# Kernel optimization log

Measured on AMD Instinct MI355X. Metric: run time of the kernel, lower is better.

## Reference

```python
import jax, jax.numpy as jnp
import numpy as np

N = 100000   # nodes
E = 1600000  # edges (before self-loops)
F_IN = 128
H = 64
G = 512      # graphs in batch


def _add_self_loops(edge_index, n):
    loop = jnp.arange(n, dtype=edge_index.dtype)
    src = jnp.concatenate([edge_index[0], loop])
    dst = jnp.concatenate([edge_index[1], loop])
    return src, dst


def _gcn_norm(src, dst, n):
    # PyG GCNConv: deg over targets with self-loops, norm = d^-1/2[src]*d^-1/2[dst]
    deg = jax.ops.segment_sum(jnp.ones_like(dst, dtype=jnp.float32), dst, num_segments=n)
    dinv = jnp.where(deg > 0, jax.lax.rsqrt(deg), 0.0)
    return dinv[src] * dinv[dst]


def _gcn_conv(x, src, dst, norm, W, b):
    xw = x @ W                                # [N, H]
    msg = xw[src] * norm[:, None]             # [E+N, H] gather + scale
    out = jax.ops.segment_sum(msg, dst, num_segments=x.shape[0])
    return out + b


def setup_inputs() -> dict:
    key = jax.random.key(0)
    ks = jax.random.split(key, 9)
    x = jax.random.normal(ks[0], (N, F_IN), dtype=jnp.float32)
    edge_index = jax.random.randint(ks[1], (2, E), 0, N, dtype=jnp.int32)
    batch = jnp.sort(jax.random.randint(ks[2], (N,), 0, G, dtype=jnp.int32))
    s1 = 1.0 / np.sqrt(F_IN)
    s2 = 1.0 / np.sqrt(H)
    W1 = jax.random.uniform(ks[3], (F_IN, H), jnp.float32, -s1, s1)
    b1 = jnp.zeros((H,), jnp.float32)
    W2 = jax.random.uniform(ks[4], (H, H), jnp.float32, -s2, s2)
    b2 = jnp.zeros((H,), jnp.float32)
    Wl = jax.random.uniform(ks[5], (H, 1), jnp.float32, -s2, s2)
    bl = jnp.zeros((1,), jnp.float32)
    return {"x": x, "edge_index": edge_index, "batch": batch,
            "W1": W1, "b1": b1, "W2": W2, "b2": b2, "Wl": Wl, "bl": bl}


def reference(x, edge_index, batch, W1, b1, W2, b2, Wl, bl):
    n = x.shape[0]
    src, dst = _add_self_loops(edge_index, n)
    norm = _gcn_norm(src, dst, n)
    h = jax.nn.relu(_gcn_conv(x, src, dst, norm, W1, b1))
    h = jax.nn.relu(_gcn_conv(h, src, dst, norm, W2, b2))
    # global mean pool over graphs
    sums = jax.ops.segment_sum(h, batch, num_segments=G)          # [G, H]
    cnt = jax.ops.segment_sum(jnp.ones((n,), jnp.float32), batch, num_segments=G)
    pooled = sums / jnp.maximum(cnt, 1.0)[:, None]
    return jax.nn.sigmoid(pooled @ Wl + bl)                        # [G, 1]
```

## Files before the change

kernel.cpp:

```cpp
#include <hip/hip_runtime.h>
#include <hip/hip_bf16.h>
#include <cmath>

#define F_IN 128
#define HDIM 64
#define NPB 128
#define NB1 512
#define CAP 2560
#define GGRID 2048

typedef __attribute__((ext_vector_type(8))) short bf16x8;
typedef __attribute__((ext_vector_type(4))) float f32x4;
typedef __attribute__((ext_vector_type(2))) float f32x2;

__device__ __forceinline__ unsigned short f2bf(float f) {
    __hip_bfloat16 h = __float2bfloat16(f);
    union { __hip_bfloat16 h; unsigned short u; } c; c.h = h; return c.u;
}
__device__ __forceinline__ unsigned char f2fp8(float f) {
    int p = __builtin_amdgcn_cvt_pk_fp8_f32(f, f, 0, false);
    return (unsigned char)(p & 0xff);
}
__device__ __forceinline__ void fp8x8_acc(uint2 v, float* a) {
    f32x2 f;
    f = __builtin_amdgcn_cvt_pk_f32_fp8(v.x, false); a[0] += f.x; a[1] += f.y;
    f = __builtin_amdgcn_cvt_pk_f32_fp8(v.x, true);  a[2] += f.x; a[3] += f.y;
    f = __builtin_amdgcn_cvt_pk_f32_fp8(v.y, false); a[4] += f.x; a[5] += f.y;
    f = __builtin_amdgcn_cvt_pk_f32_fp8(v.y, true);  a[6] += f.x; a[7] += f.y;
}

__device__ __forceinline__ void gather_rows(const int* __restrict__ col,
                                            const uint2* __restrict__ xws,
                                            int L, int s, int end, float* a) {
    int e = s;
    for (; e + 8 <= end; e += 8) {
        uint2 v0 = xws[(size_t)col[e + 0] * 8 + L];
        uint2 v1 = xws[(size_t)col[e + 1] * 8 + L];
        uint2 v2 = xws[(size_t)col[e + 2] * 8 + L];
        uint2 v3 = xws[(size_t)col[e + 3] * 8 + L];
        uint2 v4 = xws[(size_t)col[e + 4] * 8 + L];
        uint2 v5 = xws[(size_t)col[e + 5] * 8 + L];
        uint2 v6 = xws[(size_t)col[e + 6] * 8 + L];
        uint2 v7 = xws[(size_t)col[e + 7] * 8 + L];
        fp8x8_acc(v0, a); fp8x8_acc(v1, a); fp8x8_acc(v2, a); fp8x8_acc(v3, a);
        fp8x8_acc(v4, a); fp8x8_acc(v5, a); fp8x8_acc(v6, a); fp8x8_acc(v7, a);
    }
    for (; e < end; ++e)
        fp8x8_acc(xws[(size_t)col[e] * 8 + L], a);
}

__device__ __forceinline__ int remap_group(int v, int nbuk) {
    int phase = v / nbuk;
    int b = v - phase * nbuk;
    return b * 4 + (3 - phase);
}


__launch_bounds__(256)
__global__ void k_init(const float* __restrict__ W1, const float* __restrict__ W2,
                       unsigned short* __restrict__ w1t, unsigned short* __restrict__ w2t,
                       const int* __restrict__ batch, int* __restrict__ gstart,
                       int n, int G, int* __restrict__ gcnt, int nbuk,
                       float* __restrict__ pooled) {
    int t = blockIdx.x * 256 + threadIdx.x;
    if (t < F_IN * 64) {
        int c = t & 63, k = t >> 6;
        w1t[c * F_IN + k] = f2bf(W1[t]);
        return;
    }
    t -= F_IN * 64;
    if (t < HDIM * 64) {
        int c = t & 63, k = t >> 6;
        w2t[c * HDIM + k] = f2bf(W2[t]);
        return;
    }
    t -= HDIM * 64;
    if (t <= G) {
        int g = t;
        int lo = 0, hi = n;
        while (lo < hi) {
            int mid = (lo + hi) >> 1;
            if (batch[mid] < g) lo = mid + 1; else hi = mid;
        }
        gstart[g] = lo;
        return;
    }
    t -= G + 1;
    if (t < nbuk) { gcnt[t] = 0; return; }
    t -= nbuk;
    if (t < G * HDIM) pooled[t] = 0.0f;
}


__launch_bounds__(256)
__global__ void p_place(const int* __restrict__ src, const int* __restrict__ dst,
                        int* __restrict__ gcnt, int* __restrict__ pairs,
                        int E, int nbuk, int chunk) {
    __shared__ int hist[1024];
    __shared__ int cur[1024];
    int tid = threadIdx.x;
    for (int i = tid; i < nbuk; i += 256) hist[i] = 0;
    __syncthreads();
    int lo = blockIdx.x * chunk, hi = min(E, lo + chunk);
    for (int e = lo + tid; e < hi; e += 256)
        atomicAdd(&hist[dst[e] >> 7], 1);
    __syncthreads();
    for (int i = tid; i < nbuk; i += 256) {
        int c = hist[i];
        cur[i] = i * CAP + (c ? atomicAdd(&gcnt[i], c) : 0);
    }
    __syncthreads();
    for (int e = lo + tid; e < hi; e += 256) {
        int d = dst[e];
        int pos = atomicAdd(&cur[d >> 7], 1);
        pairs[pos] = (src[e] << 7) | (d & 127);
    }
}


__launch_bounds__(256)
__global__ void p2_csr(const int* __restrict__ pairs, const int* __restrict__ bucket_cnt,
                       float* __restrict__ dinv, int* __restrict__ col,
                       int4* __restrict__ slot_hdr, int n) {
    __shared__ int plds[CAP];
    __shared__ int dl[128];
    __shared__ int sc[128];
    __shared__ int cur[128];
    __shared__ int h64[64];
    __shared__ int s64[64];
    int b = blockIdx.x, tid = threadIdx.x;
    int nlo = b << 7;
    int eb = b * CAP;
    int cnt = bucket_cnt[b];
    if (tid < 128) dl[tid] = 0;
    if (tid < 64) h64[tid] = 0;
    __syncthreads();
    for (int i = tid; i < cnt; i += 256) {
        int v = pairs[eb + i];
        plds[i] = v;
        atomicAdd(&dl[v & 127], 1);
    }
    __syncthreads();
    int d0 = 0, excl = 0;
    if (tid < 128) { d0 = dl[tid]; sc[tid] = d0; }
    __syncthreads();
    for (int off = 1; off < 128; off <<= 1) {
        int a = (tid >= off && tid < 128) ? sc[tid - off] : 0;
        __syncthreads();
        if (tid < 128) sc[tid] += a;
        __syncthreads();
    }
    if (tid < 128) {
        excl = sc[tid] - d0;
        int node = nlo + tid;
        float dv = rsqrtf((float)(d0 + 1));
        if (node < n) dinv[node] = dv;
        cur[tid] = eb + excl;
        atomicAdd(&h64[min(d0, 63)], 1);
    }
    __syncthreads();
    if (tid == 0) { int run = 0; for (int i = 0; i < 64; ++i) { s64[i] = run; run += h64[i]; } }
    __syncthreads();
    if (tid < 64) h64[tid] = 0;
    __syncthreads();
    if (tid < 128) {
        int node = nlo + tid;
        int bin = min(d0, 63);
        int pos = s64[bin] + atomicAdd(&h64[bin], 1);
        int4 hdr;
        hdr.x = (node < n) ? node : 0x7fffffff;
        hdr.y = eb + excl;
        hdr.z = d0;
        hdr.w = __float_as_int(rsqrtf((float)(d0 + 1)));
        slot_hdr[nlo + pos] = hdr;
    }
    __syncthreads();
    for (int i = tid; i < cnt; i += 256) {
        unsigned int v = (unsigned int)plds[i];
        int pos = atomicAdd(&cur[v & 127], 1);
        col[pos] = (int)(v >> 7);
    }
}


template <int K>
__launch_bounds__(256)
__global__ void matmul_mfma(const float* __restrict__ X, const unsigned short* __restrict__ Wt,
                            const float* __restrict__ dinv, unsigned char* __restrict__ out,
                            int n) {
    constexpr int KS  = K / 32;
    constexpr int LDX = K + 8;
    __shared__ unsigned short Xs[64 * LDX];
    __shared__ unsigned short Ws[64 * LDX];
    int tid = threadIdx.x;
    int rowbase = blockIdx.x * 64;
    for (int i = tid; i < 64 * (K / 8); i += 256) {
        int r = i / (K / 8), ch = i % (K / 8);
        *(bf16x8*)(Ws + r * LDX + ch * 8) = ((const bf16x8*)Wt)[i];
    }
    {
        const float4* X4 = (const float4*)X;
        for (int i = tid; i < 64 * (K / 4); i += 256) {
            int r = i / (K / 4), k4 = i % (K / 4);
            ushort4 u = { 0, 0, 0, 0 };
            int gr = rowbase + r;
            if (gr < n) {
                float4 v = X4[(size_t)gr * (K / 4) + k4];
                u.x = f2bf(v.x); u.y = f2bf(v.y); u.z = f2bf(v.z); u.w = f2bf(v.w);
            }
            *(ushort4*)(Xs + r * LDX + k4 * 4) = u;
        }
    }
    __syncthreads();
    int wave = tid >> 6, lane = tid & 63;
    int q = lane >> 4, nn = lane & 15;
    f32x4 acc[4] = {{0,0,0,0},{0,0,0,0},{0,0,0,0},{0,0,0,0}};
    int mrow = wave * 16 + nn;
#pragma unroll
    for (int s = 0; s < KS; ++s) {
        bf16x8 af = *(const bf16x8*)(Xs + mrow * LDX + s * 32 + q * 8);
#pragma unroll
        for (int c = 0; c < 4; ++c) {
            bf16x8 bf = *(const bf16x8*)(Ws + (c * 16 + nn) * LDX + s * 32 + q * 8);
            acc[c] = __builtin_amdgcn_mfma_f32_16x16x32_bf16(af, bf, acc[c], 0, 0, 0);
        }
    }
#pragma unroll
    for (int r = 0; r < 4; ++r) {
        int row = rowbase + wave * 16 + q * 4 + r;
        if (row >= n) continue;
        float dv = dinv[row];
#pragma unroll
        for (int c = 0; c < 4; ++c)
            out[(size_t)row * HDIM + c * 16 + nn] = f2fp8(acc[c][r] * dv);
    }
}


__launch_bounds__(256)
__global__ void gather1_mm2(const int4* __restrict__ slot_hdr, const int* __restrict__ col,
                            const uint2* __restrict__ xws, const float* __restrict__ bias,
                            const unsigned short* __restrict__ w2t,
                            unsigned char* __restrict__ out8, int ngroups, int nbuk, int n) {
    __shared__ unsigned short Hs[32 * 72];
    __shared__ unsigned short Ws[64 * 72];
    __shared__ int   snode[32];
    __shared__ float sdinv[32];

    int tid = threadIdx.x;
    int ls = tid >> 3;
    int L  = tid & 7;

    for (int i = tid; i < 64 * 8; i += 256) {
        int r = i >> 3, ch = i & 7;
        *(bf16x8*)(Ws + r * 72 + ch * 8) = ((const bf16x8*)w2t)[i];
    }

    for (int v = blockIdx.x; v < ngroups; v += gridDim.x) {
        int grp = remap_group(v, nbuk);
        int slot = grp * 32 + ls;

        int node = 0x7fffffff;
        float dv = 0.0f;
        float a[8] = {0, 0, 0, 0, 0, 0, 0, 0};
        {
            int4 hdr = slot_hdr[slot];
            node = hdr.x;
            if (node < n) {
                dv = __int_as_float(hdr.w);
                fp8x8_acc(xws[(size_t)node * 8 + L], a);
                gather_rows(col, xws, L, hdr.y, hdr.y + hdr.z, a);
            }
        }
        if (L == 0) { snode[ls] = node; sdinv[ls] = dv; }
        {
            int f0 = L * 8;
            bf16x8 o;
            if (node < n) {
#pragma unroll
                for (int j = 0; j < 8; ++j)
                    o[j] = (short)f2bf(fmaxf(fmaf(a[j], dv, bias[f0 + j]), 0.0f));
            } else {
                short z[8] = {0,0,0,0,0,0,0,0};
                o = *(bf16x8*)z;
            }
            *(bf16x8*)(Hs + ls * 72 + L * 8) = o;
        }
        __syncthreads();

        int wave = tid >> 6, lane = tid & 63;
        int q = lane >> 4, nn = lane & 15;
        int mt  = wave & 1;
        int nt0 = (wave >> 1) * 2;
        f32x4 acc[2] = {{0,0,0,0},{0,0,0,0}};
#pragma unroll
        for (int s = 0; s < 2; ++s) {
            bf16x8 af = *(const bf16x8*)(Hs + (mt * 16 + nn) * 72 + s * 32 + q * 8);
#pragma unroll
            for (int t = 0; t < 2; ++t) {
                bf16x8 bf = *(const bf16x8*)(Ws + ((nt0 + t) * 16 + nn) * 72 + s * 32 + q * 8);
                acc[t] = __builtin_amdgcn_mfma_f32_16x16x32_bf16(af, bf, acc[t], 0, 0, 0);
            }
        }
#pragma unroll
        for (int r = 0; r < 4; ++r) {
            int lslot = mt * 16 + q * 4 + r;
            int nd = snode[lslot];
            if (nd >= n) continue;
            float dvr = sdinv[lslot];
#pragma unroll
            for (int t = 0; t < 2; ++t)
                out8[(size_t)nd * HDIM + (nt0 + t) * 16 + nn] = f2fp8(acc[t][r] * dvr);
        }
        __syncthreads();
    }
}


__launch_bounds__(256)
__global__ void gather2_pool(const int4* __restrict__ slot_hdr, const int* __restrict__ col,
                             const uint2* __restrict__ xws, const float* __restrict__ bias,
                             const int* __restrict__ batch, float* __restrict__ pooled,
                             int ngroups, int nbuk, int n, int G) {
    __shared__ float lpool[4][HDIM];
    __shared__ int sg[32];
    __shared__ int sgmin;
    int tid = threadIdx.x;
    int ls = tid >> 3;
    int L  = tid & 7;

    for (int v = blockIdx.x; v < ngroups; v += gridDim.x) {
        int grp = remap_group(v, nbuk);
        int slot = grp * 32 + ls;

        lpool[tid >> 6][tid & 63] = 0.0f;
        if (tid == 0) sgmin = 0x7fffffff;
        __syncthreads();

        int node = 0x7fffffff;
        float dv = 0.0f;
        int s = 0, deg = 0;
        {
            int4 hdr = slot_hdr[slot];
            node = hdr.x;
            if (node < n) { s = hdr.y; deg = hdr.z; dv = __int_as_float(hdr.w); }
        }
        if (L == 0) {
            int g = (node < n) ? batch[node] : 0x7fffffff;
            sg[ls] = g;
            if (node < n) atomicMin(&sgmin, g);
        }

        float a[8] = {0, 0, 0, 0, 0, 0, 0, 0};
        if (node < n) {
            fp8x8_acc(xws[(size_t)node * 8 + L], a);
            gather_rows(col, xws, L, s, s + deg, a);
        }
        __syncthreads();

        int gmin = sgmin;
        if (node < n) {
            int g  = sg[ls];
            int gl = g - gmin;
            int f0 = L * 8;
            if (gl < 4) {
#pragma unroll
                for (int j = 0; j < 8; ++j)
                    atomicAdd(&lpool[gl][f0 + j], fmaxf(fmaf(a[j], dv, bias[f0 + j]), 0.0f));
            } else {
#pragma unroll
                for (int j = 0; j < 8; ++j)
                    atomicAdd(&pooled[(size_t)g * HDIM + f0 + j],
                              fmaxf(fmaf(a[j], dv, bias[f0 + j]), 0.0f));
            }
        }
        __syncthreads();

        if (gmin != 0x7fffffff) {
            int r = tid >> 6, f = tid & 63;
            float vv = lpool[r][f];
            int gg = gmin + r;
            if (vv != 0.0f && gg < G)
                atomicAdd(&pooled[(size_t)gg * HDIM + f], vv);
        }
        __syncthreads();
    }
}


__launch_bounds__(256)
__global__ void head(const float* __restrict__ pooled, const int* __restrict__ gstart,
                     const float* __restrict__ Wl, const float* __restrict__ bl,
                     float* __restrict__ out, int G) {
    int g = blockIdx.x * 4 + (threadIdx.x >> 6);
    int f = threadIdx.x & 63;
    if (g >= G) return;
    float cnt = fmaxf((float)(gstart[g + 1] - gstart[g]), 1.0f);
    float v = pooled[(size_t)g * HDIM + f] * Wl[f] * (1.0f / cnt);
#pragma unroll
    for (int off = 32; off; off >>= 1) v += __shfl_down(v, off, 64);
    if (f == 0) out[g] = 1.0f / (1.0f + expf(-(v + bl[0])));
}


extern "C" void kernel_launch(void* const* d_in, const int* in_sizes, int n_in,
                              void* d_out, int out_size, void* d_ws, size_t ws_size,
                              hipStream_t stream) {
    const float* x   = (const float*)d_in[0];
    const int* ei    = (const int*)d_in[1];
    const int* batch = (const int*)d_in[2];
    const float* W1  = (const float*)d_in[3];
    const float* b1  = (const float*)d_in[4];
    const float* W2  = (const float*)d_in[5];
    const float* b2  = (const float*)d_in[6];
    const float* Wl  = (const float*)d_in[7];
    const float* bl  = (const float*)d_in[8];
    float* out = (float*)d_out;

    const int n = in_sizes[0] / F_IN;
    const int E = in_sizes[1] / 2;
    const int G = out_size;

    const int* srcp = ei;
    const int* dstp = ei + E;

    int nbuk = (n + NPB - 1) / NPB;
    int nslots = nbuk * NPB;
    int ngroups = nbuk * 4;

    char* wsb = (char*)d_ws;
    auto alloc = [&](size_t bytes) { char* p = wsb; wsb += (bytes + 255) & ~(size_t)255; return p; };
    float* dinv       = (float*)alloc((size_t)n * 4);
    int4*  slot_hdr   = (int4*)alloc((size_t)nslots * 16);
    int*   gcnt       = (int*)alloc(1024 * 4);
    int*   pairs      = (int*)alloc((size_t)nbuk * CAP * 4);
    int*   colx       = (int*)alloc((size_t)nbuk * CAP * 4);
    unsigned short* w1t  = (unsigned short*)alloc((size_t)F_IN * HDIM * 2);
    unsigned short* w2t  = (unsigned short*)alloc((size_t)HDIM * HDIM * 2);
    unsigned char*  xws8 = (unsigned char*)alloc((size_t)n * HDIM);
    unsigned char*  xws8b= (unsigned char*)alloc((size_t)n * HDIM);
    float* pooled     = (float*)alloc((size_t)G * HDIM * 4);
    int*   gstart     = (int*)alloc(((size_t)G + 1) * 4);

    const int TB = 256;
    int gMM  = (n + 63) / 64;
    int chunk = (E + NB1 - 1) / NB1;
    int gGat = min(GGRID, ngroups);
    int initWork = F_IN * 64 + HDIM * 64 + (G + 1) + nbuk + G * HDIM;
    int gInit = (initWork + TB - 1) / TB;

    k_init<<<gInit, TB, 0, stream>>>(W1, W2, w1t, w2t, batch, gstart, n, G,
                                     gcnt, nbuk, pooled);
    p_place<<<NB1, TB, 0, stream>>>(srcp, dstp, gcnt, pairs, E, nbuk, chunk);
    p2_csr<<<nbuk, TB, 0, stream>>>(pairs, gcnt, dinv, colx, slot_hdr, n);
    matmul_mfma<F_IN><<<gMM, TB, 0, stream>>>(x, w1t, dinv, xws8, n);
    gather1_mm2<<<gGat, TB, 0, stream>>>(slot_hdr, colx, (const uint2*)xws8,
                                         b1, w2t, xws8b, ngroups, nbuk, n);
    gather2_pool<<<gGat, TB, 0, stream>>>(slot_hdr, colx, (const uint2*)xws8b,
                                          b2, batch, pooled, ngroups, nbuk, n, G);
    head<<<(G + 3) / 4, TB, 0, stream>>>(pooled, gstart, Wl, bl, out, G);
}
```

Measured before the change: 251.6 us.

## Pad CSR rows to multiples of eight and use atomic work-stealing tickets

Pads each node's neighbor list to a multiple of eight entries, pointing the padding at a zeroed dummy row n, so the gather loop runs only unrolled 8-wide iterations with no scalar tail. It also replaces the static grid-stride loop in both gather kernels with an atomic ticket counter so blocks pull groups dynamically and balance uneven degree work. This costs extra padded loads of the dummy row, a larger col buffer, and one global atomic plus a barrier per group.

```diff
diff --git a/kernel.cpp b/kernel.cpp
--- a/kernel.cpp
+++ b/kernel.cpp
@@ -6,8 +6,11 @@
 #define HDIM 64
 #define NPB 128
 #define NB1 512
-#define CAP 2560
+#define CAP_P 2560
+#define CAP_C 3584
 #define GGRID 2048
+#define TICK1 1022
+#define TICK2 1023
 
 typedef __attribute__((ext_vector_type(8))) short bf16x8;
 typedef __attribute__((ext_vector_type(4))) float f32x4;
@@ -29,11 +32,10 @@
     f = __builtin_amdgcn_cvt_pk_f32_fp8(v.y, true);  a[6] += f.x; a[7] += f.y;
 }
 
-__device__ __forceinline__ void gather_rows(const int* __restrict__ col,
-                                            const uint2* __restrict__ xws,
-                                            int L, int s, int end, float* a) {
-    int e = s;
-    for (; e + 8 <= end; e += 8) {
+__device__ __forceinline__ void gather_rows_pad(const int* __restrict__ col,
+                                                const uint2* __restrict__ xws,
+                                                int L, int s, int end, float* a) {
+    for (int e = s; e < end; e += 8) {
         uint2 v0 = xws[(size_t)col[e + 0] * 8 + L];
         uint2 v1 = xws[(size_t)col[e + 1] * 8 + L];
         uint2 v2 = xws[(size_t)col[e + 2] * 8 + L];
@@ -45,8 +47,6 @@
         fp8x8_acc(v0, a); fp8x8_acc(v1, a); fp8x8_acc(v2, a); fp8x8_acc(v3, a);
         fp8x8_acc(v4, a); fp8x8_acc(v5, a); fp8x8_acc(v6, a); fp8x8_acc(v7, a);
     }
-    for (; e < end; ++e)
-        fp8x8_acc(xws[(size_t)col[e] * 8 + L], a);
 }
 
 __device__ __forceinline__ int remap_group(int v, int nbuk) {
@@ -60,8 +60,9 @@
 __global__ void k_init(const float* __restrict__ W1, const float* __restrict__ W2,
                        unsigned short* __restrict__ w1t, unsigned short* __restrict__ w2t,
                        const int* __restrict__ batch, int* __restrict__ gstart,
-                       int n, int G, int* __restrict__ gcnt, int nbuk,
-                       float* __restrict__ pooled) {
+                       int n, int G, int* __restrict__ gcnt,
+                       float* __restrict__ pooled,
+                       unsigned char* __restrict__ xws8, unsigned char* __restrict__ xws8b) {
     int t = blockIdx.x * 256 + threadIdx.x;
     if (t < F_IN * 64) {
         int c = t & 63, k = t >> 6;
@@ -86,9 +87,15 @@
         return;
     }
     t -= G + 1;
-    if (t < nbuk) { gcnt[t] = 0; return; }
-    t -= nbuk;
-    if (t < G * HDIM) pooled[t] = 0.0f;
+    if (t < 1024) { gcnt[t] = 0; return; }
+    t -= 1024;
+    if (t < G * HDIM) { pooled[t] = 0.0f; return; }
+    t -= G * HDIM;
+    if (t < 8) {
+        uint4 z = {0, 0, 0, 0};
+        if (t < 4) ((uint4*)(xws8  + (size_t)n * HDIM))[t]     = z;
+        else       ((uint4*)(xws8b + (size_t)n * HDIM))[t - 4] = z;
+    }
 }
 
 
@@ -107,7 +114,7 @@
     __syncthreads();
     for (int i = tid; i < nbuk; i += 256) {
         int c = hist[i];
-        cur[i] = i * CAP + (c ? atomicAdd(&gcnt[i], c) : 0);
+        cur[i] = i * CAP_P + (c ? atomicAdd(&gcnt[i], c) : 0);
     }
     __syncthreads();
     for (int e = lo + tid; e < hi; e += 256) {
@@ -122,7 +129,7 @@
 __global__ void p2_csr(const int* __restrict__ pairs, const int* __restrict__ bucket_cnt,
                        float* __restrict__ dinv, int* __restrict__ col,
                        int4* __restrict__ slot_hdr, int n) {
-    __shared__ int plds[CAP];
+    __shared__ int plds[CAP_P];
     __shared__ int dl[128];
     __shared__ int sc[128];
     __shared__ int cur[128];
@@ -130,7 +137,8 @@
     __shared__ int s64[64];
     int b = blockIdx.x, tid = threadIdx.x;
     int nlo = b << 7;
-    int eb = b * CAP;
+    int eb = b * CAP_P;
+    int cb = b * CAP_C;
     int cnt = bucket_cnt[b];
     if (tid < 128) dl[tid] = 0;
     if (tid < 64) h64[tid] = 0;
@@ -141,8 +149,8 @@
         atomicAdd(&dl[v & 127], 1);
     }
     __syncthreads();
-    int d0 = 0, excl = 0;
-    if (tid < 128) { d0 = dl[tid]; sc[tid] = d0; }
+    int d0 = 0, dp = 0, excl = 0;
+    if (tid < 128) { d0 = dl[tid]; dp = (d0 + 7) & ~7; sc[tid] = dp; }
     __syncthreads();
     for (int off = 1; off < 128; off <<= 1) {
         int a = (tid >= off && tid < 128) ? sc[tid - off] : 0;
@@ -151,12 +159,13 @@
         __syncthreads();
     }
     if (tid < 128) {
-        excl = sc[tid] - d0;
+        excl = sc[tid] - dp;
         int node = nlo + tid;
-        float dv = rsqrtf((float)(d0 + 1));
-        if (node < n) dinv[node] = dv;
-        cur[tid] = eb + excl;
+        if (node < n) dinv[node] = rsqrtf((float)(d0 + 1));
+        cur[tid] = cb + excl;
         atomicAdd(&h64[min(d0, 63)], 1);
+        for (int i = d0; i < dp; ++i)
+            col[cb + excl + i] = n;
     }
     __syncthreads();
     if (tid == 0) { int run = 0; for (int i = 0; i < 64; ++i) { s64[i] = run; run += h64[i]; } }
@@ -169,8 +178,8 @@
         int pos = s64[bin] + atomicAdd(&h64[bin], 1);
         int4 hdr;
         hdr.x = (node < n) ? node : 0x7fffffff;
-        hdr.y = eb + excl;
-        hdr.z = d0;
+        hdr.y = cb + excl;
+        hdr.z = dp;
         hdr.w = __float_as_int(rsqrtf((float)(d0 + 1)));
         slot_hdr[nlo + pos] = hdr;
     }
@@ -241,11 +250,13 @@
 __global__ void gather1_mm2(const int4* __restrict__ slot_hdr, const int* __restrict__ col,
                             const uint2* __restrict__ xws, const float* __restrict__ bias,
                             const unsigned short* __restrict__ w2t,
-                            unsigned char* __restrict__ out8, int ngroups, int nbuk, int n) {
+                            unsigned char* __restrict__ out8, int* __restrict__ ticket,
+                            int ngroups, int nbuk, int n) {
     __shared__ unsigned short Hs[32 * 72];
     __shared__ unsigned short Ws[64 * 72];
     __shared__ int   snode[32];
     __shared__ float sdinv[32];
+    __shared__ int   sv;
 
     int tid = threadIdx.x;
     int ls = tid >> 3;
@@ -256,7 +267,11 @@
         *(bf16x8*)(Ws + r * 72 + ch * 8) = ((const bf16x8*)w2t)[i];
     }
 
-    for (int v = blockIdx.x; v < ngroups; v += gridDim.x) {
+    while (true) {
+        if (tid == 0) sv = atomicAdd(ticket, 1);
+        __syncthreads();
+        int v = sv;
+        if (v >= ngroups) break;
         int grp = remap_group(v, nbuk);
         int slot = grp * 32 + ls;
 
@@ -269,7 +284,7 @@
             if (node < n) {
                 dv = __int_as_float(hdr.w);
                 fp8x8_acc(xws[(size_t)node * 8 + L], a);
-                gather_rows(col, xws, L, hdr.y, hdr.y + hdr.z, a);
+                gather_rows_pad(col, xws, L, hdr.y, hdr.y + hdr.z, a);
             }
         }
         if (L == 0) { snode[ls] = node; sdinv[ls] = dv; }
@@ -321,15 +336,20 @@
 __global__ void gather2_pool(const int4* __restrict__ slot_hdr, const int* __restrict__ col,
                              const uint2* __restrict__ xws, const float* __restrict__ bias,
                              const int* __restrict__ batch, float* __restrict__ pooled,
-                             int ngroups, int nbuk, int n, int G) {
+                             int* __restrict__ ticket, int ngroups, int nbuk, int n, int G) {
     __shared__ float lpool[4][HDIM];
     __shared__ int sg[32];
     __shared__ int sgmin;
+    __shared__ int sv;
     int tid = threadIdx.x;
     int ls = tid >> 3;
     int L  = tid & 7;
 
-    for (int v = blockIdx.x; v < ngroups; v += gridDim.x) {
+    while (true) {
+        if (tid == 0) sv = atomicAdd(ticket, 1);
+        __syncthreads();
+        int v = sv;
+        if (v >= ngroups) break;
         int grp = remap_group(v, nbuk);
         int slot = grp * 32 + ls;
 
@@ -339,11 +359,11 @@
 
         int node = 0x7fffffff;
         float dv = 0.0f;
-        int s = 0, deg = 0;
+        int s = 0, dp = 0;
         {
             int4 hdr = slot_hdr[slot];
             node = hdr.x;
-            if (node < n) { s = hdr.y; deg = hdr.z; dv = __int_as_float(hdr.w); }
+            if (node < n) { s = hdr.y; dp = hdr.z; dv = __int_as_float(hdr.w); }
         }
         if (L == 0) {
             int g = (node < n) ? batch[node] : 0x7fffffff;
@@ -354,7 +374,7 @@
         float a[8] = {0, 0, 0, 0, 0, 0, 0, 0};
         if (node < n) {
             fp8x8_acc(xws[(size_t)node * 8 + L], a);
-            gather_rows(col, xws, L, s, s + deg, a);
+            gather_rows_pad(col, xws, L, s, s + dp, a);
         }
         __syncthreads();
 
@@ -433,12 +453,12 @@
     float* dinv       = (float*)alloc((size_t)n * 4);
     int4*  slot_hdr   = (int4*)alloc((size_t)nslots * 16);
     int*   gcnt       = (int*)alloc(1024 * 4);
-    int*   pairs      = (int*)alloc((size_t)nbuk * CAP * 4);
-    int*   colx       = (int*)alloc((size_t)nbuk * CAP * 4);
+    int*   pairs      = (int*)alloc((size_t)nbuk * CAP_P * 4);
+    int*   colx       = (int*)alloc((size_t)nbuk * CAP_C * 4);
     unsigned short* w1t  = (unsigned short*)alloc((size_t)F_IN * HDIM * 2);
     unsigned short* w2t  = (unsigned short*)alloc((size_t)HDIM * HDIM * 2);
-    unsigned char*  xws8 = (unsigned char*)alloc((size_t)n * HDIM);
-    unsigned char*  xws8b= (unsigned char*)alloc((size_t)n * HDIM);
+    unsigned char*  xws8 = (unsigned char*)alloc((size_t)(n + 1) * HDIM);
+    unsigned char*  xws8b= (unsigned char*)alloc((size_t)(n + 1) * HDIM);
     float* pooled     = (float*)alloc((size_t)G * HDIM * 4);
     int*   gstart     = (int*)alloc(((size_t)G + 1) * 4);
 
@@ -446,17 +466,19 @@
     int gMM  = (n + 63) / 64;
     int chunk = (E + NB1 - 1) / NB1;
     int gGat = min(GGRID, ngroups);
-    int initWork = F_IN * 64 + HDIM * 64 + (G + 1) + nbuk + G * HDIM;
+    int initWork = F_IN * 64 + HDIM * 64 + (G + 1) + 1024 + G * HDIM + 8;
     int gInit = (initWork + TB - 1) / TB;
 
     k_init<<<gInit, TB, 0, stream>>>(W1, W2, w1t, w2t, batch, gstart, n, G,
-                                     gcnt, nbuk, pooled);
+                                     gcnt, pooled, xws8, xws8b);
     p_place<<<NB1, TB, 0, stream>>>(srcp, dstp, gcnt, pairs, E, nbuk, chunk);
     p2_csr<<<nbuk, TB, 0, stream>>>(pairs, gcnt, dinv, colx, slot_hdr, n);
     matmul_mfma<F_IN><<<gMM, TB, 0, stream>>>(x, w1t, dinv, xws8, n);
     gather1_mm2<<<gGat, TB, 0, stream>>>(slot_hdr, colx, (const uint2*)xws8,
-                                         b1, w2t, xws8b, ngroups, nbuk, n);
+                                         b1, w2t, xws8b, gcnt + TICK1,
+                                         ngroups, nbuk, n);
     gather2_pool<<<gGat, TB, 0, stream>>>(slot_hdr, colx, (const uint2*)xws8b,
-                                          b2, batch, pooled, ngroups, nbuk, n, G);
+                                          b2, batch, pooled, gcnt + TICK2,
+                                          ngroups, nbuk, n, G);
     head<<<(G + 3) / 4, TB, 0, stream>>>(pooled, gstart, Wl, bl, out, G);
 }
```

After: 309.5 us. 1.23x slower.
